# Kernel optimization log

Measured on AMD Instinct MI355X. Metric: run time of the kernel, lower is better.

The kernel has to match this reference:

```python
import jax, jax.numpy as jnp
import numpy as np

N_NODES = 100000
N_EDGES = 1600000
D_IN = 64
D_OUT = 64
E_DIM = 32
N_NODE_TYPES = 2
N_EDGE_TYPES = 3


def setup_inputs() -> dict:
    key = jax.random.key(0)
    ks = jax.random.split(key, 7)
    node_feature = jax.random.normal(ks[0], (N_NODES, D_IN), dtype=jnp.float32)
    edge_feature = jax.random.normal(ks[1], (N_EDGES, E_DIM), dtype=jnp.float32)
    # linear_node[i]: Linear(din, dout, bias=False) -> stored as [in, out]
    W_node = jax.random.normal(ks[2], (N_NODE_TYPES, D_IN, D_OUT), dtype=jnp.float32) / np.sqrt(D_IN)
    # linear_msg[i]: Linear(dout + edge_dim, dout, bias=False), msg_direction='single'
    W_msg = jax.random.normal(ks[3], (N_EDGE_TYPES, D_OUT + E_DIM, D_OUT), dtype=jnp.float32) / np.sqrt(D_OUT + E_DIM)
    node_type = jax.random.randint(ks[4], (N_NODES,), 0, N_NODE_TYPES, dtype=jnp.int32)
    edge_type = jax.random.randint(ks[5], (N_EDGES,), 0, N_EDGE_TYPES, dtype=jnp.int32)
    edge_index = jax.random.randint(ks[6], (2, N_EDGES), 0, N_NODES, dtype=jnp.int32)
    return {
        "node_feature": node_feature,
        "edge_feature": edge_feature,
        "W_node": W_node,
        "W_msg": W_msg,
        "node_type": node_type,
        "edge_type": edge_type,
        "edge_index": edge_index,
    }


def reference(node_feature, edge_feature, W_node, W_msg, node_type, edge_type, edge_index):
    # Per-node-type linear: x_out[n] = x[n] @ W_node[node_type[n]]
    # (compute per type, select by mask -- equivalent to masked gather + index_add)
    x_out = jnp.zeros((node_feature.shape[0], W_node.shape[2]), dtype=node_feature.dtype)
    for t in range(W_node.shape[0]):
        x_out = x_out + jnp.where((node_type == t)[:, None],
                                  node_feature @ W_node[t], 0.0)

    src, dst = edge_index[0], edge_index[1]
    # msg_direction == 'single': concat(x_j, edge_feature)  [E, dout+edge_dim]
    x_cat = jnp.concatenate([x_out[src], edge_feature], axis=-1)
    # Per-edge-type linear on messages
    msg = jnp.zeros((x_cat.shape[0], W_msg.shape[2]), dtype=x_cat.dtype)
    for t in range(W_msg.shape[0]):
        msg = msg + jnp.where((edge_type == t)[:, None], x_cat @ W_msg[t], 0.0)

    # normalize_adj=False -> norm is None; aggr='add' scatter into target nodes
    out = jax.ops.segment_sum(msg, dst, num_segments=node_feature.shape[0])
    return out
```

## Files before the change

kernel.cpp:

```cpp
#include <hip/hip_runtime.h>
#include <hip/hip_bf16.h>

#define N_NODES 100000
#define N_EDGES 1600000
#define D_IN 64
#define D_OUT 64
#define E_DIM 32
#define KCAT 288
#define NK (4 * N_NODES)
#define NBCHUNK 391

typedef unsigned long long u64;
typedef __hip_bfloat16 bf16;
typedef unsigned char u8;
typedef __attribute__((ext_vector_type(8))) short bf16x8v;
typedef __attribute__((ext_vector_type(4))) float f32x4v;

__device__ __forceinline__ float bflo(unsigned u) {
    union { unsigned v; float f; } x; x.v = u << 16; return x.f;
}
__device__ __forceinline__ float bfhi(unsigned u) {
    union { unsigned v; float f; } x; x.v = u & 0xffff0000u; return x.f;
}
__device__ __forceinline__ unsigned packbf2(float a, float b) {
    union { bf16 h[2]; unsigned u; } w;
    w.h[0] = __float2bfloat16(a); w.h[1] = __float2bfloat16(b);
    return w.u;
}
__device__ __forceinline__ short sbf(float f) {
    union { bf16 h; short s; } cv; cv.h = __float2bfloat16(f); return cv.s;
}

__global__ __launch_bounds__(256) void zero_buf(float4* __restrict__ p, long n4) {
    long i = (long)blockIdx.x * 256 + threadIdx.x;
    long stride = (long)gridDim.x * 256;
    float4 z = make_float4(0.f, 0.f, 0.f, 0.f);
    for (; i < n4; i += stride) p[i] = z;
}

__global__ __launch_bounds__(256) void node_xform_g(const float* __restrict__ nf,
                                                    const float* __restrict__ Wn,
                                                    const int* __restrict__ ntype,
                                                    bf16* __restrict__ xout,
                                                    int* __restrict__ cnt) {
    __shared__ float Ws[2 * 64 * 64];
    __shared__ float As[64][65];
    int tid = threadIdx.x;
    int n0 = blockIdx.x * 64;
    {
        int zi = blockIdx.x * 256 + tid;
        if (zi < NK) cnt[zi] = 0;
    }
    for (int i = tid; i < 2 * 64 * 64; i += 256) Ws[i] = Wn[i];
#pragma unroll
    for (int i = 0; i < 4; ++i) {
        int f = (i * 256 + tid) * 4;
        int r = f >> 6, c = f & 63;
        int n = n0 + r;
        float4 v = (n < N_NODES) ? *(const float4*)&nf[(size_t)n * 64 + c]
                                 : make_float4(0.f, 0.f, 0.f, 0.f);
        As[r][c + 0] = v.x; As[r][c + 1] = v.y; As[r][c + 2] = v.z; As[r][c + 3] = v.w;
    }
    __syncthreads();
    int tx = tid & 15, ty = tid >> 4;
    int r0 = n0 + ty * 4;
    int t0 = (r0 + 0 < N_NODES) ? ntype[r0 + 0] : 0;
    int t1 = (r0 + 1 < N_NODES) ? ntype[r0 + 1] : 0;
    int t2 = (r0 + 2 < N_NODES) ? ntype[r0 + 2] : 0;
    int t3 = (r0 + 3 < N_NODES) ? ntype[r0 + 3] : 0;
    float4 acc0 = {0,0,0,0}, acc1 = {0,0,0,0}, acc2 = {0,0,0,0}, acc3 = {0,0,0,0};
#pragma unroll 8
    for (int k = 0; k < 64; ++k) {
        float4 w0 = *(const float4*)&Ws[k * 64 + tx * 4];
        float4 w1 = *(const float4*)&Ws[4096 + k * 64 + tx * 4];
        float a0 = As[ty * 4 + 0][k];
        float a1 = As[ty * 4 + 1][k];
        float a2 = As[ty * 4 + 2][k];
        float a3 = As[ty * 4 + 3][k];
        float4 wa = t0 ? w1 : w0;
        float4 wb = t1 ? w1 : w0;
        float4 wc = t2 ? w1 : w0;
        float4 wd = t3 ? w1 : w0;
        acc0.x = fmaf(a0, wa.x, acc0.x); acc0.y = fmaf(a0, wa.y, acc0.y);
        acc0.z = fmaf(a0, wa.z, acc0.z); acc0.w = fmaf(a0, wa.w, acc0.w);
        acc1.x = fmaf(a1, wb.x, acc1.x); acc1.y = fmaf(a1, wb.y, acc1.y);
        acc1.z = fmaf(a1, wb.z, acc1.z); acc1.w = fmaf(a1, wb.w, acc1.w);
        acc2.x = fmaf(a2, wc.x, acc2.x); acc2.y = fmaf(a2, wc.y, acc2.y);
        acc2.z = fmaf(a2, wc.z, acc2.z); acc2.w = fmaf(a2, wc.w, acc2.w);
        acc3.x = fmaf(a3, wd.x, acc3.x); acc3.y = fmaf(a3, wd.y, acc3.y);
        acc3.z = fmaf(a3, wd.z, acc3.z); acc3.w = fmaf(a3, wd.w, acc3.w);
    }
#pragma unroll
    for (int r = 0; r < 4; ++r) {
        int n = r0 + r;
        if (n < N_NODES) {
            float4 a = (r == 0) ? acc0 : (r == 1) ? acc1 : (r == 2) ? acc2 : acc3;
            union { bf16 h[4]; uint2 u; } pk;
            pk.h[0] = __float2bfloat16(a.x); pk.h[1] = __float2bfloat16(a.y);
            pk.h[2] = __float2bfloat16(a.z); pk.h[3] = __float2bfloat16(a.w);
            *(uint2*)&xout[(size_t)n * 64 + tx * 4] = pk.u;
        }
    }
}

__global__ __launch_bounds__(256) void count_rank(const int* __restrict__ eidx,
                                                  const int* __restrict__ etype,
                                                  int* __restrict__ cnt,
                                                  int* __restrict__ krank) {
    int i = blockIdx.x * 256 + threadIdx.x;
    if (i >= N_EDGES) return;
    int d = eidx[N_EDGES + i];
    int t = etype[i];
    int key = 4 * d + t;
    int r = atomicAdd(&cnt[key], 1);
    krank[i] = (key << 8) | r;
}

__global__ __launch_bounds__(256) void scan_a(const int* __restrict__ cnt,
                                              int* __restrict__ partials) {
    __shared__ int ws[4];
    int b = blockIdx.x, tid = threadIdx.x, lane = tid & 63, wid = tid >> 6;
    int i0 = b * 1024 + tid * 4;
    int s = 0;
#pragma unroll
    for (int k = 0; k < 4; ++k) { int i = i0 + k; if (i < NK) s += cnt[i]; }
#pragma unroll
    for (int d = 32; d > 0; d >>= 1) s += __shfl_down(s, d);
    if (lane == 0) ws[wid] = s;
    __syncthreads();
    if (tid == 0) partials[b] = ws[0] + ws[1] + ws[2] + ws[3];
}

__global__ __launch_bounds__(256) void scan_c(const int* __restrict__ cnt,
                                              const int* __restrict__ partials,
                                              int* __restrict__ offs) {
    __shared__ int sp[512];
    __shared__ int wsum[4];
    int tid = threadIdx.x;
    sp[tid]       = (tid < NBCHUNK) ? partials[tid] : 0;
    sp[tid + 256] = (tid + 256 < NBCHUNK) ? partials[tid + 256] : 0;
    __syncthreads();
    for (int d = 1; d < 512; d <<= 1) {
        int u0 = (tid >= d) ? sp[tid - d] : 0;
        int u1 = sp[tid + 256 - d];
        __syncthreads();
        sp[tid] += u0; sp[tid + 256] += u1;
        __syncthreads();
    }
    int b = blockIdx.x;
    int pex = (b == 0) ? 0 : sp[b - 1];

    int lane = tid & 63, wid = tid >> 6;
    int i0 = b * 1024 + tid * 4;
    int c0 = (i0 + 0 < NK) ? cnt[i0 + 0] : 0;
    int c1 = (i0 + 1 < NK) ? cnt[i0 + 1] : 0;
    int c2 = (i0 + 2 < NK) ? cnt[i0 + 2] : 0;
    int c3 = (i0 + 3 < NK) ? cnt[i0 + 3] : 0;
    int lsum = c0 + c1 + c2 + c3;
    int v = lsum;
#pragma unroll
    for (int d = 1; d < 64; d <<= 1) {
        int u = __shfl_up(v, d);
        if (lane >= d) v += u;
    }
    int wexcl = v - lsum;
    if (lane == 63) wsum[wid] = v;
    __syncthreads();
    int bexcl = 0;
    for (int w = 0; w < wid; ++w) bexcl += wsum[w];
    int base = pex + bexcl + wexcl;
    if (i0 + 0 < NK) offs[i0 + 0] = base; base += c0;
    if (i0 + 1 < NK) offs[i0 + 1] = base; base += c1;
    if (i0 + 2 < NK) offs[i0 + 2] = base; base += c2;
    if (i0 + 3 < NK) offs[i0 + 3] = base;
}

__global__ __launch_bounds__(256) void place_pay(const int* __restrict__ eidx,
                                                 const int* __restrict__ krank,
                                                 const int* __restrict__ offs,
                                                 u64* __restrict__ pay) {
    int i = blockIdx.x * 256 + threadIdx.x;
    if (i >= N_EDGES) return;
    int kr = krank[i];
    int key = (int)((unsigned)kr >> 8);
    int r = kr & 255;
    int s = eidx[i];
    int pos = offs[key] + r;
    pay[pos] = (u64)(unsigned)s | ((u64)(unsigned)i << 32);
}

__global__ __launch_bounds__(256) void aggregate_g(const u64* __restrict__ pay,
                                                   const int* __restrict__ offs,
                                                   const bf16* __restrict__ xout,
                                                   const float* __restrict__ ef,
                                                   bf16* __restrict__ B) {
    int wid = threadIdx.x >> 6, lane = threadIdx.x & 63;
    int gw = blockIdx.x * 4 + wid, nw = gridDim.x * 4;
    int c = lane & 31, half = lane >> 5;
    int h4 = half << 2;
    const unsigned* xo32 = (const unsigned*)xout;
    if (gw >= N_NODES) return;

    int4 o = ((const int4*)offs)[gw];
    u64 p = 0ull;
    {
        int beg = __builtin_amdgcn_readfirstlane(o.x);
        int end = __builtin_amdgcn_readfirstlane(o.w);
        if (beg + lane < end) p = pay[beg + lane];
    }

    for (int n = gw; n < N_NODES; n += nw) {
        int nn = n + nw;
        int4 onext = make_int4(0, 0, 0, 0);
        u64 pnext = 0ull;
        if (nn < N_NODES) {
            onext = ((const int4*)offs)[nn];
            int nbeg = __builtin_amdgcn_readfirstlane(onext.x);
            int nend = __builtin_amdgcn_readfirstlane(onext.w);
            if (nbeg + lane < nend) pnext = pay[nbeg + lane];
        }
        int beg = __builtin_amdgcn_readfirstlane(o.x);
        int y   = __builtin_amdgcn_readfirstlane(o.y);
        int z   = __builtin_amdgcn_readfirstlane(o.z);
        int end = __builtin_amdgcn_readfirstlane(o.w);
        float2 xa = make_float2(0.f, 0.f), xb = make_float2(0.f, 0.f), xc = make_float2(0.f, 0.f);
        float ea = 0.f, eb = 0.f, ec = 0.f;

        u64 pcur = p;
        for (int base = beg; base < end; base += 64) {
            int m = end - base; if (m > 64) m = 64;
            if (base != beg) pcur = (lane < m) ? pay[base + lane] : 0ull;
            int plo = (int)(unsigned)pcur;
            int phi = (int)(unsigned)(pcur >> 32);
            for (int j = 0; j < m; j += 16) {
                int sgp[8], egp[8];
#pragma unroll
                for (int q = 0; q < 8; ++q) {
                    int baddr = ((j + 2 * q) << 2) + h4;
                    sgp[q] = __builtin_amdgcn_ds_bpermute(baddr, plo);
                    egp[q] = __builtin_amdgcn_ds_bpermute(baddr, phi);
                }
                unsigned xv[8];
                float evv[8];
#pragma unroll
                for (int q = 0; q < 8; ++q) {
                    xv[q]  = xo32[(unsigned)sgp[q] * 32u + (unsigned)c];
                    evv[q] = ef[(unsigned)egp[q] * 32u + (unsigned)c];
                }
#pragma unroll
                for (int q = 0; q < 8; ++q) {
                    float2 x2v = make_float2(bflo(xv[q]), bfhi(xv[q]));
                    float ev = evv[q];
                    int i0 = base + j + 2 * q;
                    if (i0 + 1 < y) {
                        xa.x += x2v.x; xa.y += x2v.y; ea += ev;
                    } else if (i0 >= y && i0 + 1 < z) {
                        xb.x += x2v.x; xb.y += x2v.y; eb += ev;
                    } else if (i0 >= z && i0 + 1 < end) {
                        xc.x += x2v.x; xc.y += x2v.y; ec += ev;
                    } else {
                        int idx = i0 + half;
                        bool v = idx < end;
                        float fl = v ? x2v.x : 0.f, fh = v ? x2v.y : 0.f, fe = v ? ev : 0.f;
                        if (idx < y)      { xa.x += fl; xa.y += fh; ea += fe; }
                        else if (idx < z) { xb.x += fl; xb.y += fh; eb += fe; }
                        else              { xc.x += fl; xc.y += fh; ec += fe; }
                    }
                }
            }
        }
        xa.x += __shfl_down(xa.x, 32); xa.y += __shfl_down(xa.y, 32);
        xb.x += __shfl_down(xb.x, 32); xb.y += __shfl_down(xb.y, 32);
        xc.x += __shfl_down(xc.x, 32); xc.y += __shfl_down(xc.y, 32);
        ea   += __shfl_down(ea, 32);   eb   += __shfl_down(eb, 32);   ec += __shfl_down(ec, 32);

        if (lane < 32) {
            bf16* Bn = B + (size_t)n * KCAT;
            *(unsigned*)&Bn[2 * c]       = packbf2(xa.x, xa.y);
            *(unsigned*)&Bn[64 + 2 * c]  = packbf2(xb.x, xb.y);
            *(unsigned*)&Bn[128 + 2 * c] = packbf2(xc.x, xc.y);
            Bn[192 + c] = __float2bfloat16(ea);
            Bn[224 + c] = __float2bfloat16(eb);
            Bn[256 + c] = __float2bfloat16(ec);
        }
        o = onext;
        p = pnext;
    }
}

__global__ __launch_bounds__(256) void final_gemm_mfma(const bf16* __restrict__ Bb,
                                                       const float* __restrict__ Wm,
                                                       float* __restrict__ out) {
    __shared__ short WT[64][312];
    int tid = threadIdx.x;
#pragma unroll
    for (int i = 0; i < 18; ++i) {
        int ch = i * 256 + tid;
        int r  = ch >> 4;
        int j0 = (ch & 15) * 4;
        int t, kin;
        if (r < 192) { t = r >> 6; kin = r & 63; }
        else         { int s2 = r - 192; t = s2 >> 5; kin = 64 + (s2 & 31); }
        float4 v = *(const float4*)&Wm[(t * 96 + kin) * 64 + j0];
        WT[j0 + 0][r] = sbf(v.x);
        WT[j0 + 1][r] = sbf(v.y);
        WT[j0 + 2][r] = sbf(v.z);
        WT[j0 + 3][r] = sbf(v.w);
    }
    __syncthreads();

    int w = tid >> 6, l = tid & 63;
    int lrow = l & 15;
    int lk = (l >> 4) * 8;
    int nbase = blockIdx.x * 64 + w * 16;
    int node = nbase + lrow;
    int nodec = (node < N_NODES) ? node : (N_NODES - 1);
    const bf16* arow = Bb + (size_t)nodec * KCAT + lk;
    f32x4v acc0 = {0.f, 0.f, 0.f, 0.f}, acc1 = acc0, acc2 = acc0, acc3 = acc0;
#pragma unroll
    for (int kk = 0; kk < 9; ++kk) {
        bf16x8v a  = *(const bf16x8v*)(arow + kk * 32);
        bf16x8v b0 = *(const bf16x8v*)&WT[ 0 + lrow][kk * 32 + lk];
        bf16x8v b1 = *(const bf16x8v*)&WT[16 + lrow][kk * 32 + lk];
        bf16x8v b2 = *(const bf16x8v*)&WT[32 + lrow][kk * 32 + lk];
        bf16x8v b3 = *(const bf16x8v*)&WT[48 + lrow][kk * 32 + lk];
        acc0 = __builtin_amdgcn_mfma_f32_16x16x32_bf16(a, b0, acc0, 0, 0, 0);
        acc1 = __builtin_amdgcn_mfma_f32_16x16x32_bf16(a, b1, acc1, 0, 0, 0);
        acc2 = __builtin_amdgcn_mfma_f32_16x16x32_bf16(a, b2, acc2, 0, 0, 0);
        acc3 = __builtin_amdgcn_mfma_f32_16x16x32_bf16(a, b3, acc3, 0, 0, 0);
    }
    int col = l & 15;
    int row0 = (l >> 4) * 4;
#pragma unroll
    for (int r = 0; r < 4; ++r) {
        int n = nbase + row0 + r;
        if (n < N_NODES) {
            float* on = out + (size_t)n * 64;
            on[ 0 + col] = acc0[r];
            on[16 + col] = acc1[r];
            on[32 + col] = acc2[r];
            on[48 + col] = acc3[r];
        }
    }
}

__global__ __launch_bounds__(256) void fallback_edge(const float* __restrict__ nf,
                                                     const float* __restrict__ ef,
                                                     const float* __restrict__ Wn,
                                                     const float* __restrict__ Wm,
                                                     const int* __restrict__ ntype,
                                                     const int* __restrict__ etype,
                                                     const int* __restrict__ eidx,
                                                     float* __restrict__ out) {
    __shared__ float wn[2 * 64 * 64];
    __shared__ float wm[3 * 96 * 64];
    for (int i = threadIdx.x; i < 2 * 64 * 64; i += 256) wn[i] = Wn[i];
    for (int i = threadIdx.x; i < 3 * 96 * 64; i += 256) wm[i] = Wm[i];
    __syncthreads();
    int wid = threadIdx.x >> 6, lane = threadIdx.x & 63;
    for (int e = blockIdx.x * 4 + wid; e < N_EDGES; e += gridDim.x * 4) {
        int t = etype[e];
        int s = eidx[e];
        int d = eidx[N_EDGES + e];
        int nt = ntype[s];
        float xs = nf[(long)s * 64 + lane];
        const float* wcol = &wn[nt * 4096 + lane];
        float xo = 0.f;
#pragma unroll 16
        for (int k = 0; k < 64; ++k) xo = fmaf(__shfl(xs, k), wcol[k * 64], xo);
        float ev = ef[(long)e * 32 + (lane & 31)];
        const float* mcol = &wm[t * 96 * 64 + lane];
        float m = 0.f;
#pragma unroll 16
        for (int k = 0; k < 64; ++k) m = fmaf(__shfl(xo, k), mcol[k * 64], m);
#pragma unroll 8
        for (int k = 0; k < 32; ++k) m = fmaf(__shfl(ev, k), mcol[(64 + k) * 64], m);
        atomicAdd(&out[(long)d * 64 + lane], m);
    }
}

extern "C" void kernel_launch(void* const* d_in, const int* in_sizes, int n_in,
                              void* d_out, int out_size, void* d_ws, size_t ws_size,
                              hipStream_t stream) {
    const float* nf    = (const float*)d_in[0];
    const float* ef    = (const float*)d_in[1];
    const float* Wn    = (const float*)d_in[2];
    const float* Wm    = (const float*)d_in[3];
    const int*   ntype = (const int*)d_in[4];
    const int*   etype = (const int*)d_in[5];
    const int*   eidx  = (const int*)d_in[6];
    float* out = (float*)d_out;

    const size_t xout_bytes = (size_t)N_NODES * 64 * 2;
    const size_t b_bytes    = (size_t)N_NODES * KCAT * 2;

    if (ws_size >= xout_bytes + b_bytes) {
        bf16* xout = (bf16*)d_ws;
        bf16* B    = (bf16*)((char*)d_ws + xout_bytes);
        u64* pay      = (u64*)d_out;
        int* cnt      = (int*)(pay + N_EDGES);
        int* offs     = cnt + NK;
        int* partials = offs + NK;
        int* krank    = partials + 512;

        node_xform_g<<<(N_NODES + 63) / 64, 256, 0, stream>>>(nf, Wn, ntype, xout, cnt);
        count_rank<<<(N_EDGES + 255) / 256, 256, 0, stream>>>(eidx, etype, cnt, krank);
        scan_a<<<NBCHUNK, 256, 0, stream>>>(cnt, partials);
        scan_c<<<NBCHUNK, 256, 0, stream>>>(cnt, partials, offs);
        place_pay<<<(N_EDGES + 255) / 256, 256, 0, stream>>>(eidx, krank, offs, pay);
        aggregate_g<<<4096, 256, 0, stream>>>(pay, offs, xout, ef, B);
        final_gemm_mfma<<<(N_NODES + 63) / 64, 256, 0, stream>>>(B, Wm, out);
    } else {
        zero_buf<<<2048, 256, 0, stream>>>((float4*)d_out, (long)((size_t)out_size * 4 / 16));
        fallback_edge<<<4096, 256, 0, stream>>>(nf, ef, Wn, Wm, ntype, etype, eidx, out);
    }
}
```

Measured before the change: 255.5 us.

## Fuse counting sort phases into one persistent kernel with grid barriers

Replaces the four separate sort kernels (count/rank, two scan passes, placement) with a single persistent kernel of 512 blocks that synchronises through software grid barriers. Edge keys, ranks and sources stay in registers across phases, which removes the krank round trip through global memory and three kernel launches. It relies on all 512 blocks being co-resident for the spin barrier; without cooperative launch this could deadlock if occupancy were insufficient, and the barrier spin adds atomic traffic.

```diff
diff --git a/kernel.cpp b/kernel.cpp
--- a/kernel.cpp
+++ b/kernel.cpp
@@ -9,6 +9,9 @@
 #define KCAT 288
 #define NK (4 * N_NODES)
 #define NBCHUNK 391
+#define SORT_BLOCKS 512
+#define SORT_STRIDE (SORT_BLOCKS * 256)
+#define SORT_ITER ((N_EDGES + SORT_STRIDE - 1) / SORT_STRIDE)
 
 typedef unsigned long long u64;
 typedef __hip_bfloat16 bf16;
@@ -31,6 +34,22 @@
     union { bf16 h; short s; } cv; cv.h = __float2bfloat16(f); return cv.s;
 }
 
+__device__ __forceinline__ void grid_sync(int* cntp, int* genp) {
+    __threadfence();
+    __syncthreads();
+    if (threadIdx.x == 0) {
+        int g = __hip_atomic_load(genp, __ATOMIC_ACQUIRE, __HIP_MEMORY_SCOPE_AGENT);
+        int arrived = __hip_atomic_fetch_add(cntp, 1, __ATOMIC_ACQ_REL, __HIP_MEMORY_SCOPE_AGENT);
+        if (arrived == SORT_BLOCKS - 1) {
+            __hip_atomic_store(cntp, 0, __ATOMIC_RELAXED, __HIP_MEMORY_SCOPE_AGENT);
+            __hip_atomic_store(genp, g + 1, __ATOMIC_RELEASE, __HIP_MEMORY_SCOPE_AGENT);
+        } else {
+            while (__hip_atomic_load(genp, __ATOMIC_ACQUIRE, __HIP_MEMORY_SCOPE_AGENT) == g) {}
+        }
+    }
+    __syncthreads();
+}
+
 __global__ __launch_bounds__(256) void zero_buf(float4* __restrict__ p, long n4) {
     long i = (long)blockIdx.x * 256 + threadIdx.x;
     long stride = (long)gridDim.x * 256;
@@ -42,7 +61,8 @@
                                                     const float* __restrict__ Wn,
                                                     const int* __restrict__ ntype,
                                                     bf16* __restrict__ xout,
-                                                    int* __restrict__ cnt) {
+                                                    int* __restrict__ cnt,
+                                                    int* __restrict__ bar) {
     __shared__ float Ws[2 * 64 * 64];
     __shared__ float As[64][65];
     int tid = threadIdx.x;
@@ -50,6 +70,7 @@
     {
         int zi = blockIdx.x * 256 + tid;
         if (zi < NK) cnt[zi] = 0;
+        if (blockIdx.x == 0 && tid < 2) bar[tid] = 0;
     }
     for (int i = tid; i < 2 * 64 * 64; i += 256) Ws[i] = Wn[i];
 #pragma unroll
@@ -103,90 +124,95 @@
     }
 }
 
-__global__ __launch_bounds__(256) void count_rank(const int* __restrict__ eidx,
-                                                  const int* __restrict__ etype,
-                                                  int* __restrict__ cnt,
-                                                  int* __restrict__ krank) {
-    int i = blockIdx.x * 256 + threadIdx.x;
-    if (i >= N_EDGES) return;
-    int d = eidx[N_EDGES + i];
-    int t = etype[i];
-    int key = 4 * d + t;
-    int r = atomicAdd(&cnt[key], 1);
-    krank[i] = (key << 8) | r;
-}
-
-__global__ __launch_bounds__(256) void scan_a(const int* __restrict__ cnt,
-                                              int* __restrict__ partials) {
-    __shared__ int ws[4];
-    int b = blockIdx.x, tid = threadIdx.x, lane = tid & 63, wid = tid >> 6;
-    int i0 = b * 1024 + tid * 4;
-    int s = 0;
-#pragma unroll
-    for (int k = 0; k < 4; ++k) { int i = i0 + k; if (i < NK) s += cnt[i]; }
-#pragma unroll
-    for (int d = 32; d > 0; d >>= 1) s += __shfl_down(s, d);
-    if (lane == 0) ws[wid] = s;
-    __syncthreads();
-    if (tid == 0) partials[b] = ws[0] + ws[1] + ws[2] + ws[3];
-}
-
-__global__ __launch_bounds__(256) void scan_c(const int* __restrict__ cnt,
-                                              const int* __restrict__ partials,
-                                              int* __restrict__ offs) {
+__global__ __launch_bounds__(256, 2) void sort_coop(const int* __restrict__ eidx,
+                                                    const int* __restrict__ etype,
+                                                    int* __restrict__ cnt,
+                                                    int* __restrict__ partials,
+                                                    int* __restrict__ offs,
+                                                    u64* __restrict__ pay,
+                                                    int* __restrict__ bar) {
     __shared__ int sp[512];
     __shared__ int wsum[4];
+    __shared__ int ws4[4];
     int tid = threadIdx.x;
-    sp[tid]       = (tid < NBCHUNK) ? partials[tid] : 0;
-    sp[tid + 256] = (tid + 256 < NBCHUNK) ? partials[tid + 256] : 0;
-    __syncthreads();
-    for (int d = 1; d < 512; d <<= 1) {
-        int u0 = (tid >= d) ? sp[tid - d] : 0;
-        int u1 = sp[tid + 256 - d];
+    int base = blockIdx.x * 256 + tid;
+
+    int key[SORT_ITER], rk[SORT_ITER], src[SORT_ITER];
+#pragma unroll
+    for (int q = 0; q < SORT_ITER; ++q) {
+        int i = base + q * SORT_STRIDE;
+        key[q] = -1; rk[q] = 0; src[q] = 0;
+        if (i < N_EDGES) {
+            int d = eidx[N_EDGES + i];
+            int t = etype[i];
+            key[q] = 4 * d + t;
+            src[q] = eidx[i];
+            rk[q] = atomicAdd(&cnt[key[q]], 1);
+        }
+    }
+    grid_sync(&bar[0], &bar[1]);
+
+    if (blockIdx.x < NBCHUNK) {
+        int lane = tid & 63, wid = tid >> 6;
+        int i0 = blockIdx.x * 1024 + tid * 4;
+        int s = 0;
+#pragma unroll
+        for (int k = 0; k < 4; ++k) { int i = i0 + k; if (i < NK) s += cnt[i]; }
+#pragma unroll
+        for (int d = 32; d > 0; d >>= 1) s += __shfl_down(s, d);
+        if (lane == 0) ws4[wid] = s;
         __syncthreads();
-        sp[tid] += u0; sp[tid + 256] += u1;
+        if (tid == 0) partials[blockIdx.x] = ws4[0] + ws4[1] + ws4[2] + ws4[3];
+    }
+    grid_sync(&bar[0], &bar[1]);
+
+    if (blockIdx.x < NBCHUNK) {
+        sp[tid]       = (tid < NBCHUNK) ? partials[tid] : 0;
+        sp[tid + 256] = (tid + 256 < NBCHUNK) ? partials[tid + 256] : 0;
         __syncthreads();
-    }
-    int b = blockIdx.x;
-    int pex = (b == 0) ? 0 : sp[b - 1];
-
-    int lane = tid & 63, wid = tid >> 6;
-    int i0 = b * 1024 + tid * 4;
-    int c0 = (i0 + 0 < NK) ? cnt[i0 + 0] : 0;
-    int c1 = (i0 + 1 < NK) ? cnt[i0 + 1] : 0;
-    int c2 = (i0 + 2 < NK) ? cnt[i0 + 2] : 0;
-    int c3 = (i0 + 3 < NK) ? cnt[i0 + 3] : 0;
-    int lsum = c0 + c1 + c2 + c3;
-    int v = lsum;
-#pragma unroll
-    for (int d = 1; d < 64; d <<= 1) {
-        int u = __shfl_up(v, d);
-        if (lane >= d) v += u;
-    }
-    int wexcl = v - lsum;
-    if (lane == 63) wsum[wid] = v;
-    __syncthreads();
-    int bexcl = 0;
-    for (int w = 0; w < wid; ++w) bexcl += wsum[w];
-    int base = pex + bexcl + wexcl;
-    if (i0 + 0 < NK) offs[i0 + 0] = base; base += c0;
-    if (i0 + 1 < NK) offs[i0 + 1] = base; base += c1;
-    if (i0 + 2 < NK) offs[i0 + 2] = base; base += c2;
-    if (i0 + 3 < NK) offs[i0 + 3] = base;
-}
-
-__global__ __launch_bounds__(256) void place_pay(const int* __restrict__ eidx,
-                                                 const int* __restrict__ krank,
-                                                 const int* __restrict__ offs,
-                                                 u64* __restrict__ pay) {
-    int i = blockIdx.x * 256 + threadIdx.x;
-    if (i >= N_EDGES) return;
-    int kr = krank[i];
-    int key = (int)((unsigned)kr >> 8);
-    int r = kr & 255;
-    int s = eidx[i];
-    int pos = offs[key] + r;
-    pay[pos] = (u64)(unsigned)s | ((u64)(unsigned)i << 32);
+        for (int d = 1; d < 512; d <<= 1) {
+            int u0 = (tid >= d) ? sp[tid - d] : 0;
+            int u1 = sp[tid + 256 - d];
+            __syncthreads();
+            sp[tid] += u0; sp[tid + 256] += u1;
+            __syncthreads();
+        }
+        int b = blockIdx.x;
+        int pex = (b == 0) ? 0 : sp[b - 1];
+        int lane = tid & 63, wid = tid >> 6;
+        int i0 = b * 1024 + tid * 4;
+        int c0 = (i0 + 0 < NK) ? cnt[i0 + 0] : 0;
+        int c1 = (i0 + 1 < NK) ? cnt[i0 + 1] : 0;
+        int c2 = (i0 + 2 < NK) ? cnt[i0 + 2] : 0;
+        int c3 = (i0 + 3 < NK) ? cnt[i0 + 3] : 0;
+        int lsum = c0 + c1 + c2 + c3;
+        int v = lsum;
+#pragma unroll
+        for (int d = 1; d < 64; d <<= 1) {
+            int u = __shfl_up(v, d);
+            if (lane >= d) v += u;
+        }
+        int wexcl = v - lsum;
+        if (lane == 63) wsum[wid] = v;
+        __syncthreads();
+        int bexcl = 0;
+        for (int w = 0; w < wid; ++w) bexcl += wsum[w];
+        int basep = pex + bexcl + wexcl;
+        if (i0 + 0 < NK) offs[i0 + 0] = basep; basep += c0;
+        if (i0 + 1 < NK) offs[i0 + 1] = basep; basep += c1;
+        if (i0 + 2 < NK) offs[i0 + 2] = basep; basep += c2;
+        if (i0 + 3 < NK) offs[i0 + 3] = basep;
+    }
+    grid_sync(&bar[0], &bar[1]);
+
+#pragma unroll
+    for (int q = 0; q < SORT_ITER; ++q) {
+        if (key[q] >= 0) {
+            int i = base + q * SORT_STRIDE;
+            int pos = offs[key[q]] + rk[q];
+            pay[pos] = (u64)(unsigned)src[q] | ((u64)(unsigned)i << 32);
+        }
+    }
 }
 
 __global__ __launch_bounds__(256) void aggregate_g(const u64* __restrict__ pay,
@@ -401,13 +427,10 @@
         int* cnt      = (int*)(pay + N_EDGES);
         int* offs     = cnt + NK;
         int* partials = offs + NK;
-        int* krank    = partials + 512;
-
-        node_xform_g<<<(N_NODES + 63) / 64, 256, 0, stream>>>(nf, Wn, ntype, xout, cnt);
-        count_rank<<<(N_EDGES + 255) / 256, 256, 0, stream>>>(eidx, etype, cnt, krank);
-        scan_a<<<NBCHUNK, 256, 0, stream>>>(cnt, partials);
-        scan_c<<<NBCHUNK, 256, 0, stream>>>(cnt, partials, offs);
-        place_pay<<<(N_EDGES + 255) / 256, 256, 0, stream>>>(eidx, krank, offs, pay);
+        int* bar      = partials + 500;
+
+        node_xform_g<<<(N_NODES + 63) / 64, 256, 0, stream>>>(nf, Wn, ntype, xout, cnt, bar);
+        sort_coop<<<SORT_BLOCKS, 256, 0, stream>>>(eidx, etype, cnt, partials, offs, pay, bar);
         aggregate_g<<<4096, 256, 0, stream>>>(pay, offs, xout, ef, B);
         final_gemm_mfma<<<(N_NODES + 63) / 64, 256, 0, stream>>>(B, Wm, out);
     } else {
```

Result: slower. 487.8 us (+90.9%).
